# Performance work log

Hardware: AMD Instinct MI355X
Metric: run time of the kernel (lower is better)

The kernel has to match this reference:

```python
import jax, jax.numpy as jnp
import numpy as np

B, T = 64, 500000

def setup_inputs() -> dict:
    key = jax.random.key(0)
    k1, k2 = jax.random.split(key)
    input_attenuation = jax.random.normal(k1, (B, T), dtype=jnp.float32)
    input_wet_dry = jax.random.randint(k2, (B, T), 0, 2).astype(jnp.bool_)
    return {"input_attenuation": input_attenuation, "input_wet_dry": input_wet_dry}

def reference(input_attenuation, input_wet_dry):
    # baseline[i] = baseline[i-1] if wet[i] else attenuation[i]; baseline[0] = attenuation[0].
    # Equivalent to gathering attenuation at the most recent 'dry' index (index 0 forced dry).
    Bn, Tn = input_attenuation.shape
    t = jnp.arange(Tn, dtype=jnp.int32)
    dry = jnp.logical_not(input_wet_dry).at[:, 0].set(True)  # timestep 0 always uses attenuation[0]
    pos = jnp.where(dry, t[None, :], jnp.int32(-1))          # [B, T]
    idx = jax.lax.associative_scan(jnp.maximum, pos, axis=1)  # running max = last dry index
    return jnp.take_along_axis(input_attenuation, idx, axis=1)
```

## Files before the change

kernel.cpp:

```cpp
#include <hip/hip_runtime.h>

__global__ __launch_bounds__(256) void ffill_kernel(
    const float* __restrict__ att,
    const int* __restrict__ wet,
    float* __restrict__ out,
    int T, int chunkElems)
{
    const int r    = blockIdx.y;
    const int c    = blockIdx.x;
    const int tid  = threadIdx.x;
    const int lane = tid & 63;
    const int w    = tid >> 6;
    const long long rowBase = (long long)r * T;
    const int base = c * chunkElems;

    __shared__ float s_wave_val[4];
    __shared__ int   s_wave_has[4];
    __shared__ float s_block_carry;

    const int e = base + tid * 4;
    const bool valid = (e < T);
    float4 a = make_float4(0.f, 0.f, 0.f, 0.f);
    int4 wv = make_int4(1, 1, 1, 1);
    if (valid) {
        a  = *reinterpret_cast<const float4*>(att + rowBase + e);
        wv = *reinterpret_cast<const int4*>(wet + rowBase + e);
    }

    if (tid < 64) {
        float carry = 0.0f;
        int hi = base;
        while (hi > 0) {
            const int start = (hi >= 64) ? (hi - 64) : 0;
            const int idx   = start + lane;
            bool dry = false;
            if (idx < hi) {
                dry = (wet[rowBase + idx] == 0) || (idx == 0);
            }
            const unsigned long long m = __ballot(dry);
            if (m != 0ull) {
                const int src = 63 - __clzll(m);
                if (lane == 0) carry = att[rowBase + start + src];
                break;
            }
            hi = start;
        }
        if (lane == 0) s_block_carry = carry;
    }

    bool d0 = (wv.x == 0);
    bool d1 = (wv.y == 0);
    bool d2 = (wv.z == 0);
    bool d3 = (wv.w == 0);
    if (e == 0) d0 = true;
    if (!valid) { d0 = d1 = d2 = d3 = false; }

    const bool has = d0 | d1 | d2 | d3;
    const float lastval = d3 ? a.w : (d2 ? a.z : (d1 ? a.y : a.x));

    const unsigned long long mask = __ballot(has);
    const int src = (mask != 0ull) ? (63 - __clzll(mask)) : 0;
    const float wval = __shfl(lastval, src);
    if (lane == 0) {
        s_wave_has[w] = (mask != 0ull) ? 1 : 0;
        s_wave_val[w] = wval;
    }
    __syncthreads();

    float carry_in = s_block_carry;
    #pragma unroll
    for (int ww = 0; ww < 4; ++ww) {
        if (ww < w && s_wave_has[ww]) carry_in = s_wave_val[ww];
    }
    const unsigned long long pm = mask & ((1ull << lane) - 1ull);
    const int psrc = (pm != 0ull) ? (63 - __clzll(pm)) : 0;
    const float pval = __shfl(lastval, psrc);
    if (pm != 0ull) carry_in = pval;

    if (valid) {
        float running = carry_in;
        float4 o;
        running = d0 ? a.x : running;  o.x = running;
        running = d1 ? a.y : running;  o.y = running;
        running = d2 ? a.z : running;  o.z = running;
        running = d3 ? a.w : running;  o.w = running;
        *reinterpret_cast<float4*>(out + rowBase + e) = o;
    }
}

extern "C" void kernel_launch(void* const* d_in, const int* in_sizes, int n_in,
                              void* d_out, int out_size, void* d_ws, size_t ws_size,
                              hipStream_t stream) {
    const float* att = (const float*)d_in[0];
    const int* wet   = (const int*)d_in[1];
    float* out       = (float*)d_out;

    const int B = 64;
    const int T = in_sizes[0] / B;
    const int chunkElems = 1024;
    const int chunks = (T + chunkElems - 1) / chunkElems;

    dim3 grid(chunks, B);
    dim3 block(256);
    ffill_kernel<<<grid, block, 0, stream>>>(att, wet, out, T, chunkElems);
}
```

Before: 291.9 us.

## Give each wave a 4096-element segment with sequential carry and prefetch

Each wavefront now owns an independent 4096-element segment instead of each block handling 1024 elements. The wave walks it in 16 steps of 256 elements, carrying the last dry value from one step to the next in a register and prefetching the next step's loads. This removes the shared-memory cross-wave combine and __syncthreads, and cuts the number of backward carry searches by a factor of four. The cost is less memory-level parallelism per wave, with fewer loads in flight, and a longer serial chain inside each wave.

```diff
diff --git a/kernel.cpp b/kernel.cpp
--- a/kernel.cpp
+++ b/kernel.cpp
@@ -1,90 +1,92 @@
 #include <hip/hip_runtime.h>
 
-__global__ __launch_bounds__(256) void ffill_kernel(
+
+constexpr int WSEG   = 4096;
+constexpr int WCHUNK = 256;
+constexpr int WITERS = WSEG / WCHUNK;
+
+__global__ __launch_bounds__(256) void ffill_wave_kernel(
     const float* __restrict__ att,
     const int* __restrict__ wet,
     float* __restrict__ out,
-    int T, int chunkElems)
+    int T, int segsPerRow)
 {
+    const int lane = threadIdx.x & 63;
+    const int wid  = threadIdx.x >> 6;
+    const int s    = blockIdx.x * 4 + wid;
+    if (s >= segsPerRow) return;
     const int r    = blockIdx.y;
-    const int c    = blockIdx.x;
-    const int tid  = threadIdx.x;
-    const int lane = tid & 63;
-    const int w    = tid >> 6;
     const long long rowBase = (long long)r * T;
-    const int base = c * chunkElems;
+    const int base = s * WSEG;
 
-    __shared__ float s_wave_val[4];
-    __shared__ int   s_wave_has[4];
-    __shared__ float s_block_carry;
+    float carry = 0.0f;
+    int hi = base;
+    while (hi > 0) {
+        const int start = (hi >= 64) ? (hi - 64) : 0;
+        const int idx   = start + lane;
+        bool dry = false;
+        if (idx < hi) dry = (wet[rowBase + idx] == 0) || (idx == 0);
+        const unsigned long long m = __ballot(dry);
+        if (m != 0ull) {
+            const int src = 63 - __clzll(m);
+            carry = att[rowBase + start + src];
+            break;
+        }
+        hi = start;
+    }
 
-    const int e = base + tid * 4;
-    const bool valid = (e < T);
+    int e = base + lane * 4;
+    bool valid = (e < T);
     float4 a = make_float4(0.f, 0.f, 0.f, 0.f);
-    int4 wv = make_int4(1, 1, 1, 1);
+    int4  wv = make_int4(1, 1, 1, 1);
     if (valid) {
         a  = *reinterpret_cast<const float4*>(att + rowBase + e);
         wv = *reinterpret_cast<const int4*>(wet + rowBase + e);
     }
 
-    if (tid < 64) {
-        float carry = 0.0f;
-        int hi = base;
-        while (hi > 0) {
-            const int start = (hi >= 64) ? (hi - 64) : 0;
-            const int idx   = start + lane;
-            bool dry = false;
-            if (idx < hi) {
-                dry = (wet[rowBase + idx] == 0) || (idx == 0);
+    for (int it = 0; it < WITERS; ++it) {
+        float4 a_n = make_float4(0.f, 0.f, 0.f, 0.f);
+        int4  wv_n = make_int4(1, 1, 1, 1);
+        bool valid_n = false;
+        if (it + 1 < WITERS) {
+            const int en = e + WCHUNK;
+            valid_n = (en < T);
+            if (valid_n) {
+                a_n  = *reinterpret_cast<const float4*>(att + rowBase + en);
+                wv_n = *reinterpret_cast<const int4*>(wet + rowBase + en);
             }
-            const unsigned long long m = __ballot(dry);
-            if (m != 0ull) {
-                const int src = 63 - __clzll(m);
-                if (lane == 0) carry = att[rowBase + start + src];
-                break;
-            }
-            hi = start;
         }
-        if (lane == 0) s_block_carry = carry;
-    }
 
-    bool d0 = (wv.x == 0);
-    bool d1 = (wv.y == 0);
-    bool d2 = (wv.z == 0);
-    bool d3 = (wv.w == 0);
-    if (e == 0) d0 = true;
-    if (!valid) { d0 = d1 = d2 = d3 = false; }
+        bool d0 = (wv.x == 0) || (e == 0);
+        bool d1 = (wv.y == 0);
+        bool d2 = (wv.z == 0);
+        bool d3 = (wv.w == 0);
+        if (!valid) { d0 = d1 = d2 = d3 = false; }
 
-    const bool has = d0 | d1 | d2 | d3;
-    const float lastval = d3 ? a.w : (d2 ? a.z : (d1 ? a.y : a.x));
+        const bool has = d0 | d1 | d2 | d3;
+        const float lastval = d3 ? a.w : (d2 ? a.z : (d1 ? a.y : a.x));
 
-    const unsigned long long mask = __ballot(has);
-    const int src = (mask != 0ull) ? (63 - __clzll(mask)) : 0;
-    const float wval = __shfl(lastval, src);
-    if (lane == 0) {
-        s_wave_has[w] = (mask != 0ull) ? 1 : 0;
-        s_wave_val[w] = wval;
-    }
-    __syncthreads();
+        const unsigned long long mask = __ballot(has);
+        const unsigned long long pm = mask & ((1ull << lane) - 1ull);
+        const int psrc = (pm != 0ull) ? (63 - __clzll(pm)) : 0;
+        const float pval = __shfl(lastval, psrc);
+        const float carry_in = (pm != 0ull) ? pval : carry;
 
-    float carry_in = s_block_carry;
-    #pragma unroll
-    for (int ww = 0; ww < 4; ++ww) {
-        if (ww < w && s_wave_has[ww]) carry_in = s_wave_val[ww];
-    }
-    const unsigned long long pm = mask & ((1ull << lane) - 1ull);
-    const int psrc = (pm != 0ull) ? (63 - __clzll(pm)) : 0;
-    const float pval = __shfl(lastval, psrc);
-    if (pm != 0ull) carry_in = pval;
+        if (valid) {
+            float running = carry_in;
+            float4 o;
+            running = d0 ? a.x : running;  o.x = running;
+            running = d1 ? a.y : running;  o.y = running;
+            running = d2 ? a.z : running;  o.z = running;
+            running = d3 ? a.w : running;  o.w = running;
+            *reinterpret_cast<float4*>(out + rowBase + e) = o;
+        }
 
-    if (valid) {
-        float running = carry_in;
-        float4 o;
-        running = d0 ? a.x : running;  o.x = running;
-        running = d1 ? a.y : running;  o.y = running;
-        running = d2 ? a.z : running;  o.z = running;
-        running = d3 ? a.w : running;  o.w = running;
-        *reinterpret_cast<float4*>(out + rowBase + e) = o;
+        const int wsrc = (mask != 0ull) ? (63 - __clzll(mask)) : 0;
+        const float wval = __shfl(lastval, wsrc);
+        if (mask != 0ull) carry = wval;
+
+        a = a_n; wv = wv_n; valid = valid_n; e += WCHUNK;
     }
 }
 
@@ -97,10 +99,10 @@
 
     const int B = 64;
     const int T = in_sizes[0] / B;
-    const int chunkElems = 1024;
-    const int chunks = (T + chunkElems - 1) / chunkElems;
+    const int segsPerRow = (T + WSEG - 1) / WSEG;
+    const int blocksX = (segsPerRow + 3) / 4;
 
-    dim3 grid(chunks, B);
+    dim3 grid(blocksX, B);
     dim3 block(256);
-    ffill_kernel<<<grid, block, 0, stream>>>(att, wet, out, T, chunkElems);
+    ffill_wave_kernel<<<grid, block, 0, stream>>>(att, wet, out, T, segsPerRow);
 }
```

New measurement: 308.0 us. 1.06x slower.
